# Performance work log

Hardware: AMD Instinct MI355X
Metric: run time of the kernel (lower is better)

## Reference

```python
import jax, jax.numpy as jnp
import numpy as np

N = 4096      # num nodes
F = 64        # input feature dim
H = 8         # head_num
D = 8         # att_embedding_size


def setup_inputs() -> dict:
    key = jax.random.key(0)
    k1, k2, k3, k4, k5, k6 = jax.random.split(key, 6)
    X = jax.random.normal(k1, (N, F), dtype=jnp.float32)
    # sparse-ish binary adjacency with self loops (avg degree ~ 41)
    A = (jax.random.uniform(k2, (N, N)) < 0.01).astype(jnp.float32)
    A = jnp.maximum(A, jnp.eye(N, dtype=jnp.float32))
    # glorot-uniform-ish parameter init
    lim_w = np.sqrt(6.0 / (F + H * D)).astype(np.float32)
    W = jax.random.uniform(k3, (F, H * D), minval=-lim_w, maxval=lim_w, dtype=jnp.float32)
    lim_a = np.sqrt(6.0 / (1 + H * D)).astype(np.float32)
    att_self = jax.random.uniform(k4, (H, D), minval=-lim_a, maxval=lim_a, dtype=jnp.float32)
    att_neigh = jax.random.uniform(k5, (H, D), minval=-lim_a, maxval=lim_a, dtype=jnp.float32)
    bias = jnp.zeros((H, D), dtype=jnp.float32)
    return {"X": X, "A": A, "W": W, "att_self": att_self, "att_neigh": att_neigh, "bias": bias}


def reference(X, A, W, att_self, att_neigh, bias):
    # features: [N, H, D]
    feats = (X @ W).reshape(-1, H, D)
    # additive attention logits per node/head: [N, H]
    a_self = jnp.einsum('nhd,hd->nh', feats, att_self)
    a_neigh = jnp.einsum('nhd,hd->nh', feats, att_neigh)
    # scores[h, i, j] = a_self[i, h] + a_neigh[j, h]  -> [H, N, N]
    scores = a_self.T[:, :, None] + a_neigh.T[:, None, :]
    scores = jax.nn.leaky_relu(scores, negative_slope=0.2)
    # adjacency mask: -1e10 where no edge
    scores = scores + (-1e10 * (1.0 - A))[None, :, :]
    attn = jax.nn.softmax(scores, axis=-1)           # [H, N, N]
    # aggregate: [H, N, N] x [N, H, D] -> [N, H, D]
    out = jnp.einsum('hij,jhd->ihd', attn, feats)
    out = out + bias[None, :, :]                     # use_bias
    out = out.reshape(-1, H * D)                     # reduction='concat'
    return jax.nn.relu(out)                          # activation=relu
```

## Files before the change

kernel.cpp:

```cpp
#include <hip/hip_runtime.h>
#include <hip/hip_bf16.h>

#define NNODES 4096
#define NF 64
#define NH 8
#define ND 8
#define HD 64
#define ESTRIDE 4096

__device__ __forceinline__ float ldv(const void* p, int i, bool f32) {
    return f32 ? ((const float*)p)[i]
               : __bfloat162float(((const __hip_bfloat16*)p)[i]);
}

__device__ __forceinline__ void ld8(const void* base, int idx, bool f32, float* o) {
    if (f32) {
        const float4* p = (const float4*)((const float*)base + idx);
        float4 a = p[0], b = p[1];
        o[0]=a.x; o[1]=a.y; o[2]=a.z; o[3]=a.w;
        o[4]=b.x; o[5]=b.y; o[6]=b.z; o[7]=b.w;
    } else {
        uint4 u = *(const uint4*)((const unsigned short*)base + idx);
        unsigned int ws[4] = {u.x, u.y, u.z, u.w};
        #pragma unroll
        for (int q = 0; q < 4; ++q) {
            o[2*q]   = __uint_as_float(ws[q] << 16);
            o[2*q+1] = __uint_as_float(ws[q] & 0xffff0000u);
        }
    }
}

__device__ __forceinline__ bool a_is_f32(const void* A) {
    return *(const unsigned int*)A == 0x3F800000u;
}

__global__ __launch_bounds__(256) void gat_feats(
    const void* __restrict__ X,
    const void* __restrict__ W,
    const void* __restrict__ att_self,
    const void* __restrict__ att_neigh,
    const void* __restrict__ A,
    float* __restrict__ feats,
    float* __restrict__ a_self,
    float* __restrict__ a_neigh)
{
    const bool f32 = a_is_f32(A);
    __shared__ float Wl[NF][HD];
    __shared__ float Xl[4][NF];

    const int t = threadIdx.x;

    {
        float wv[16];
        ld8(W, t * 16,     f32, wv);
        ld8(W, t * 16 + 8, f32, wv + 8);
        const int row = t >> 2, col0 = (t & 3) * 16;
        #pragma unroll
        for (int k = 0; k < 16; ++k) Wl[row][col0 + k] = wv[k];
    }
    if (t < 32) {
        const int row = t >> 3, col = (t & 7) * 8;
        float xv[8];
        ld8(X, (blockIdx.x * 4 + row) * NF + col, f32, xv);
        #pragma unroll
        for (int k = 0; k < 8; ++k) Xl[row][col + k] = xv[k];
    }
    __syncthreads();

    const int r = t >> 6;
    const int c = t & 63;

    float acc = 0.f;
    #pragma unroll
    for (int k = 0; k < NF; ++k)
        acc = fmaf(Xl[r][k], Wl[k][c], acc);

    const int n = blockIdx.x * 4 + r;
    feats[n * HD + c] = acc;

    const int d = c & 7;
    const int h = c >> 3;
    float vs = acc * ldv(att_self, c, f32);
    float vn = acc * ldv(att_neigh, c, f32);
    #pragma unroll
    for (int off = 1; off < 8; off <<= 1) {
        vs += __shfl_xor(vs, off, 64);
        vn += __shfl_xor(vn, off, 64);
    }
    if (d == 0) {
        a_self[n * NH + h]  = vs;
        a_neigh[n * NH + h] = vn;
    }
}

__global__ __launch_bounds__(256) void gat_scan(
    const void* __restrict__ A,
    unsigned short* __restrict__ elist_g,
    int* __restrict__ ecnt)
{
    const int i = blockIdx.x;
    const int t = threadIdx.x;
    const bool f32 = a_is_f32(A);
    const int wave = t >> 6, lane = t & 63;
    __shared__ int wtot[4];

    unsigned int bits = 0;
    if (f32) {
        const uint4* ap = (const uint4*)((const float*)A + (size_t)i * NNODES + t * 16);
        #pragma unroll
        for (int q = 0; q < 4; ++q) {
            uint4 p = ap[q];
            if (p.x) bits |= 1u << (4 * q + 0);
            if (p.y) bits |= 1u << (4 * q + 1);
            if (p.z) bits |= 1u << (4 * q + 2);
            if (p.w) bits |= 1u << (4 * q + 3);
        }
    } else {
        const uint4* ap = (const uint4*)((const unsigned short*)A + (size_t)i * NNODES + t * 16);
        uint4 p0 = ap[0], p1 = ap[1];
        unsigned int w0[4] = {p0.x, p0.y, p0.z, p0.w};
        unsigned int w1[4] = {p1.x, p1.y, p1.z, p1.w};
        #pragma unroll
        for (int q = 0; q < 4; ++q) {
            if (w0[q] & 0x0000ffffu) bits |= 1u << (2 * q);
            if (w0[q] & 0xffff0000u) bits |= 1u << (2 * q + 1);
            if (w1[q] & 0x0000ffffu) bits |= 1u << (8 + 2 * q);
            if (w1[q] & 0xffff0000u) bits |= 1u << (8 + 2 * q + 1);
        }
    }

    int cnt = __popc(bits);
    int incl = cnt;
    #pragma unroll
    for (int off = 1; off < 64; off <<= 1) {
        int nn = __shfl_up(incl, off, 64);
        if (lane >= off) incl += nn;
    }
    if (lane == 63) wtot[wave] = incl;
    __syncthreads();
    int base = 0;
    #pragma unroll
    for (int w = 0; w < 4; ++w) if (w < wave) base += wtot[w];

    int off0 = i * ESTRIDE + base + (incl - cnt);
    unsigned int mb = bits;
    while (mb) {
        int b = __ffs(mb) - 1; mb &= mb - 1;
        elist_g[off0++] = (unsigned short)(t * 16 + b);
    }
    if (t == 0) ecnt[i] = wtot[0] + wtot[1] + wtot[2] + wtot[3];
}

__global__ __launch_bounds__(256) void gat_aggr(
    const unsigned short* __restrict__ elist_g,
    const int* __restrict__ ecnt,
    const float* __restrict__ feats,
    const float* __restrict__ a_self_g,
    const float* __restrict__ a_neigh,
    const void* __restrict__ bias,
    const void* __restrict__ A,
    float* __restrict__ out)
{
    const bool f32 = a_is_f32(A);
    const int wave = threadIdx.x >> 6, lane = threadIdx.x & 63;
    const int i = (blockIdx.x << 2) + wave;
    const int c = lane, h = lane >> 3;

    const float ash = a_self_g[i * NH + h];
    const int nE = ecnt[i];
    const unsigned short* el = elist_g + (size_t)i * ESTRIDE;

    float acc = 0.f, den = 0.f;
    int e = 0;

    if (nE >= 8) {
        uint4 ev = *(const uint4*)el;
        for (; e + 8 <= nE; e += 8) {
            uint4 nx = (e + 16 <= nE) ? *(const uint4*)(el + e + 8) : ev;
            int j[8];
            j[0] = ev.x & 0xffff; j[1] = ev.x >> 16;
            j[2] = ev.y & 0xffff; j[3] = ev.y >> 16;
            j[4] = ev.z & 0xffff; j[5] = ev.z >> 16;
            j[6] = ev.w & 0xffff; j[7] = ev.w >> 16;
            float an[8], fv[8];
            #pragma unroll
            for (int k = 0; k < 8; ++k) an[k] = a_neigh[j[k] * NH + h];
            #pragma unroll
            for (int k = 0; k < 8; ++k) fv[k] = feats[j[k] * HD + c];
            #pragma unroll
            for (int k = 0; k < 8; ++k) {
                float s = ash + an[k];
                s = (s >= 0.f) ? s : 0.2f * s;
                float wt = __expf(s);
                acc = fmaf(wt, fv[k], acc);
                den += wt;
            }
            ev = nx;
        }
    }
    for (; e < nE; ++e) {
        int j = el[e];
        float s = ash + a_neigh[j * NH + h];
        s = (s >= 0.f) ? s : 0.2f * s;
        float wt = __expf(s);
        acc = fmaf(wt, feats[j * HD + c], acc);
        den += wt;
    }

    float v = acc / den + ldv(bias, c, f32);
    out[(size_t)i * HD + c] = fmaxf(v, 0.f);
}

extern "C" void kernel_launch(void* const* d_in, const int* in_sizes, int n_in,
                              void* d_out, int out_size, void* d_ws, size_t ws_size,
                              hipStream_t stream) {
    const void* X         = d_in[0];
    const void* A         = d_in[1];
    const void* W         = d_in[2];
    const void* att_self  = d_in[3];
    const void* att_neigh = d_in[4];
    const void* bias      = d_in[5];
    float* out = (float*)d_out;

    float* feats   = (float*)d_ws;
    float* a_self  = feats  + NNODES * HD;
    float* a_neigh = a_self + NNODES * NH;
    int*   ecnt    = (int*)(a_neigh + NNODES * NH);
    unsigned short* elist = (unsigned short*)(ecnt + NNODES);

    gat_feats<<<NNODES / 4, 256, 0, stream>>>(X, W, att_self, att_neigh, A,
                                              feats, a_self, a_neigh);
    gat_scan<<<NNODES, 256, 0, stream>>>(A, elist, ecnt);
    gat_aggr<<<NNODES / 4, 256, 0, stream>>>(elist, ecnt, feats, a_self,
                                             a_neigh, bias, A, out);
}
```

Baseline: 33.36 us.

## Fuse adjacency scan into aggregation kernel with per-wave LDS edge lists

Removes the separate scan kernel. Each wave now scans its own adjacency row with a 64-bit mask per lane and compacts neighbor indices into shared memory, then aggregates directly from that list. This drops a kernel launch and the global edge-list and count round trip. The aggregation loop is also unrolled to 16 edges with a 4-edge tail. In exchange, 32KB of LDS per block may reduce occupancy, and each lane now reads a strided 64-element chunk of the row.

New measurement: 33.42 us. Within noise of the previous version (+0.2%).

```diff
diff --git a/kernel.cpp b/kernel.cpp
--- a/kernel.cpp
+++ b/kernel.cpp
@@ -6,7 +6,8 @@
 #define NH 8
 #define ND 8
 #define HD 64
-#define ESTRIDE 4096
+
+typedef unsigned long long u64;
 
 __device__ __forceinline__ float ldv(const void* p, int i, bool f32) {
     return f32 ? ((const float*)p)[i]
@@ -93,109 +94,111 @@
     }
 }
 
-__global__ __launch_bounds__(256) void gat_scan(
+__global__ __launch_bounds__(256) void gat_aggr(
     const void* __restrict__ A,
-    unsigned short* __restrict__ elist_g,
-    int* __restrict__ ecnt)
+    const float* __restrict__ feats,
+    const float* __restrict__ a_self_g,
+    const float* __restrict__ a_neigh,
+    const void* __restrict__ bias,
+    float* __restrict__ out)
 {
-    const int i = blockIdx.x;
-    const int t = threadIdx.x;
     const bool f32 = a_is_f32(A);
-    const int wave = t >> 6, lane = t & 63;
-    __shared__ int wtot[4];
-
-    unsigned int bits = 0;
+    const int wid = threadIdx.x >> 6, lane = threadIdx.x & 63;
+    const int i = (blockIdx.x << 2) + wid;
+
+    __shared__ unsigned short els[4][NNODES];
+    unsigned short* el = els[wid];
+
+    u64 bits = 0;
     if (f32) {
-        const uint4* ap = (const uint4*)((const float*)A + (size_t)i * NNODES + t * 16);
-        #pragma unroll
-        for (int q = 0; q < 4; ++q) {
+        const uint4* ap = (const uint4*)((const float*)A + (size_t)i * NNODES + lane * 64);
+        #pragma unroll
+        for (int half = 0; half < 2; ++half) {
+            unsigned int mw = 0;
+            #pragma unroll
+            for (int q = 0; q < 8; ++q) {
+                uint4 p = ap[half * 8 + q];
+                if (p.x) mw |= 1u << (4 * q + 0);
+                if (p.y) mw |= 1u << (4 * q + 1);
+                if (p.z) mw |= 1u << (4 * q + 2);
+                if (p.w) mw |= 1u << (4 * q + 3);
+            }
+            bits |= (u64)mw << (32 * half);
+        }
+    } else {
+        const uint4* ap = (const uint4*)((const unsigned short*)A + (size_t)i * NNODES + lane * 64);
+        #pragma unroll
+        for (int q = 0; q < 8; ++q) {
             uint4 p = ap[q];
-            if (p.x) bits |= 1u << (4 * q + 0);
-            if (p.y) bits |= 1u << (4 * q + 1);
-            if (p.z) bits |= 1u << (4 * q + 2);
-            if (p.w) bits |= 1u << (4 * q + 3);
-        }
-    } else {
-        const uint4* ap = (const uint4*)((const unsigned short*)A + (size_t)i * NNODES + t * 16);
-        uint4 p0 = ap[0], p1 = ap[1];
-        unsigned int w0[4] = {p0.x, p0.y, p0.z, p0.w};
-        unsigned int w1[4] = {p1.x, p1.y, p1.z, p1.w};
-        #pragma unroll
-        for (int q = 0; q < 4; ++q) {
-            if (w0[q] & 0x0000ffffu) bits |= 1u << (2 * q);
-            if (w0[q] & 0xffff0000u) bits |= 1u << (2 * q + 1);
-            if (w1[q] & 0x0000ffffu) bits |= 1u << (8 + 2 * q);
-            if (w1[q] & 0xffff0000u) bits |= 1u << (8 + 2 * q + 1);
-        }
-    }
-
-    int cnt = __popc(bits);
+            unsigned int w[4] = {p.x, p.y, p.z, p.w};
+            #pragma unroll
+            for (int r = 0; r < 4; ++r) {
+                int b = q * 8 + r * 2;
+                if (w[r] & 0x0000ffffu) bits |= 1ull << b;
+                if (w[r] & 0xffff0000u) bits |= 1ull << (b + 1);
+            }
+        }
+    }
+
+    int cnt = __popcll(bits);
     int incl = cnt;
     #pragma unroll
     for (int off = 1; off < 64; off <<= 1) {
         int nn = __shfl_up(incl, off, 64);
         if (lane >= off) incl += nn;
     }
-    if (lane == 63) wtot[wave] = incl;
+    const int nE = __shfl(incl, 63, 64);
+    int off0 = incl - cnt;
+    u64 mb = bits;
+    while (mb) {
+        int b = __ffsll(mb) - 1; mb &= mb - 1;
+        el[off0++] = (unsigned short)(lane * 64 + b);
+    }
     __syncthreads();
-    int base = 0;
-    #pragma unroll
-    for (int w = 0; w < 4; ++w) if (w < wave) base += wtot[w];
-
-    int off0 = i * ESTRIDE + base + (incl - cnt);
-    unsigned int mb = bits;
-    while (mb) {
-        int b = __ffs(mb) - 1; mb &= mb - 1;
-        elist_g[off0++] = (unsigned short)(t * 16 + b);
-    }
-    if (t == 0) ecnt[i] = wtot[0] + wtot[1] + wtot[2] + wtot[3];
-}
-
-__global__ __launch_bounds__(256) void gat_aggr(
-    const unsigned short* __restrict__ elist_g,
-    const int* __restrict__ ecnt,
-    const float* __restrict__ feats,
-    const float* __restrict__ a_self_g,
-    const float* __restrict__ a_neigh,
-    const void* __restrict__ bias,
-    const void* __restrict__ A,
-    float* __restrict__ out)
-{
-    const bool f32 = a_is_f32(A);
-    const int wave = threadIdx.x >> 6, lane = threadIdx.x & 63;
-    const int i = (blockIdx.x << 2) + wave;
+
     const int c = lane, h = lane >> 3;
-
     const float ash = a_self_g[i * NH + h];
-    const int nE = ecnt[i];
-    const unsigned short* el = elist_g + (size_t)i * ESTRIDE;
-
     float acc = 0.f, den = 0.f;
     int e = 0;
 
-    if (nE >= 8) {
-        uint4 ev = *(const uint4*)el;
-        for (; e + 8 <= nE; e += 8) {
-            uint4 nx = (e + 16 <= nE) ? *(const uint4*)(el + e + 8) : ev;
-            int j[8];
-            j[0] = ev.x & 0xffff; j[1] = ev.x >> 16;
-            j[2] = ev.y & 0xffff; j[3] = ev.y >> 16;
-            j[4] = ev.z & 0xffff; j[5] = ev.z >> 16;
-            j[6] = ev.w & 0xffff; j[7] = ev.w >> 16;
-            float an[8], fv[8];
-            #pragma unroll
-            for (int k = 0; k < 8; ++k) an[k] = a_neigh[j[k] * NH + h];
-            #pragma unroll
-            for (int k = 0; k < 8; ++k) fv[k] = feats[j[k] * HD + c];
-            #pragma unroll
-            for (int k = 0; k < 8; ++k) {
-                float s = ash + an[k];
-                s = (s >= 0.f) ? s : 0.2f * s;
-                float wt = __expf(s);
-                acc = fmaf(wt, fv[k], acc);
-                den += wt;
-            }
-            ev = nx;
+    for (; e + 16 <= nE; e += 16) {
+        uint4 e0 = *(const uint4*)(el + e);
+        uint4 e1 = *(const uint4*)(el + e + 8);
+        int j[16];
+        j[0]=e0.x&0xffff; j[1]=e0.x>>16; j[2]=e0.y&0xffff; j[3]=e0.y>>16;
+        j[4]=e0.z&0xffff; j[5]=e0.z>>16; j[6]=e0.w&0xffff; j[7]=e0.w>>16;
+        j[8]=e1.x&0xffff; j[9]=e1.x>>16; j[10]=e1.y&0xffff; j[11]=e1.y>>16;
+        j[12]=e1.z&0xffff; j[13]=e1.z>>16; j[14]=e1.w&0xffff; j[15]=e1.w>>16;
+        float an[16], fv[16];
+        #pragma unroll
+        for (int k = 0; k < 16; ++k) an[k] = a_neigh[j[k] * NH + h];
+        #pragma unroll
+        for (int k = 0; k < 16; ++k) fv[k] = feats[j[k] * HD + c];
+        #pragma unroll
+        for (int k = 0; k < 16; ++k) {
+            float s = ash + an[k];
+            s = (s >= 0.f) ? s : 0.2f * s;
+            float wt = __expf(s);
+            acc = fmaf(wt, fv[k], acc);
+            den += wt;
+        }
+    }
+    for (; e + 4 <= nE; e += 4) {
+        uint2 ee = *(const uint2*)(el + e);
+        int j[4];
+        j[0]=ee.x&0xffff; j[1]=ee.x>>16; j[2]=ee.y&0xffff; j[3]=ee.y>>16;
+        float an[4], fv[4];
+        #pragma unroll
+        for (int k = 0; k < 4; ++k) an[k] = a_neigh[j[k] * NH + h];
+        #pragma unroll
+        for (int k = 0; k < 4; ++k) fv[k] = feats[j[k] * HD + c];
+        #pragma unroll
+        for (int k = 0; k < 4; ++k) {
+            float s = ash + an[k];
+            s = (s >= 0.f) ? s : 0.2f * s;
+            float wt = __expf(s);
+            acc = fmaf(wt, fv[k], acc);
+            den += wt;
         }
     }
     for (; e < nE; ++e) {
@@ -225,12 +228,8 @@
     float* feats   = (float*)d_ws;
     float* a_self  = feats  + NNODES * HD;
     float* a_neigh = a_self + NNODES * NH;
-    int*   ecnt    = (int*)(a_neigh + NNODES * NH);
-    unsigned short* elist = (unsigned short*)(ecnt + NNODES);
 
     gat_feats<<<NNODES / 4, 256, 0, stream>>>(X, W, att_self, att_neigh, A,
                                               feats, a_self, a_neigh);
-    gat_scan<<<NNODES, 256, 0, stream>>>(A, elist, ecnt);
-    gat_aggr<<<NNODES / 4, 256, 0, stream>>>(elist, ecnt, feats, a_self,
-                                             a_neigh, bias, A, out);
-}
+    gat_aggr<<<NNODES / 4, 256, 0, stream>>>(A, feats, a_self, a_neigh, bias, out);
+}
```
